# Kernel tuning notes

Hardware: AMD Instinct MI355X
Metric: run time of the kernel (lower is better)

## Reference

```python
import jax, jax.numpy as jnp
import numpy as np

H = 2        # num_heads
C = 128      # in_channels
K_ORDER = 4
BETA = 0.5


def _gcn_conv(x, row, col, deg_inv, n):
    # x: [N, H, C]; adj_t = D^{-1} A^T where A[row, col] = 1
    # (adj_t @ x)[c] = deg_inv[c] * sum_{e: col_e == c} x[row_e]
    msg = x[row]  # [E, H, C]
    agg = jax.ops.segment_sum(msg, col, num_segments=n)  # [N, H, C]
    return agg * deg_inv[:, None, None]


def _attn_conv(qs, ks, vs):
    # linear (kernelized) attention, non-block path
    n = qs.shape[0]
    kvs = jnp.einsum('lhm,lhd->hmd', ks, vs)            # [H, C, C]
    qkvs = jnp.einsum('nhm,hmd->nhd', qs, kvs)          # [N, H, C]
    vs_sum = vs.sum(axis=0)                             # [H, C]
    num = qkvs + vs_sum[None, :, :]
    ks_sum = ks.sum(axis=0)                             # [H, C]
    qks_sum = jnp.einsum('nhm,hm->nh', qs, ks_sum)[:, :, None]  # [N, H, 1]
    den = qks_sum + jnp.asarray(n, qs.dtype)
    return num / den


def setup_inputs() -> dict:
    key = jax.random.key(0)
    ks = jax.random.split(key, 8)
    N, E = 100000, 1600000
    x = jax.random.normal(ks[0], (N, C), jnp.float32)
    edge_index = jax.random.randint(ks[1], (2, E), 0, N, jnp.int64)
    s_in = 1.0 / np.sqrt(C)
    s_out = 1.0 / np.sqrt(H * C * (K_ORDER + 1))
    Wq_w = jax.random.normal(ks[2], (C, H * C), jnp.float32) * s_in
    Wq_b = jax.random.normal(ks[3], (H * C,), jnp.float32) * s_in
    Wk_w = jax.random.normal(ks[4], (C, H * C), jnp.float32) * s_in
    Wk_b = jax.random.normal(ks[5], (H * C,), jnp.float32) * s_in
    Wo_w = jax.random.normal(ks[6], (H * C * (K_ORDER + 1), C), jnp.float32) * s_out
    Wo_b = jax.random.normal(ks[7], (C,), jnp.float32) * s_out
    return {"x": x, "edge_index": edge_index, "Wq_w": Wq_w, "Wq_b": Wq_b,
            "Wk_w": Wk_w, "Wk_b": Wk_b, "Wo_w": Wo_w, "Wo_b": Wo_b}


def reference(x, edge_index, Wq_w, Wq_b, Wk_w, Wk_b, Wo_w, Wo_b):
    n = x.shape[0]
    row, col = edge_index[0], edge_index[1]
    # normalized adjacency D^{-1} A^T (pow(-1.0) in the source, not -0.5)
    deg = jax.ops.segment_sum(jnp.ones(row.shape[0], x.dtype), col, num_segments=n)
    deg_inv = jnp.where(deg > 0, 1.0 / deg, 0.0)

    query = (x @ Wq_w + Wq_b).reshape(n, H, C)
    key = (x @ Wk_w + Wk_b).reshape(n, H, C)
    qs = query / jnp.linalg.norm(query, axis=2, keepdims=True)
    ks = key / jnp.linalg.norm(key, axis=2, keepdims=True)

    x0 = jnp.broadcast_to(x[:, None, :], (n, H, C))  # [N, H, C]
    terms = [x0]
    for _ in range(K_ORDER):
        prev = terms[-1]
        gcn_i = _gcn_conv(prev, row, col, deg_inv, n)
        attn_i = _attn_conv(qs, ks, prev)
        terms.append(BETA * gcn_i + attn_i)
    xcat = jnp.concatenate(terms, axis=-1)  # [N, H, C*(K+1)]
    xcat = xcat.reshape(n, H * C * (K_ORDER + 1))
    return (xcat @ Wo_w + Wo_b) / H
```

## Files before the change

### kernel.cpp

```cpp
#include <hip/hip_runtime.h>

#define THREADS 256
#define NB 512
#define SEGCAP 6144

typedef __attribute__((ext_vector_type(8))) short short8;
typedef __attribute__((ext_vector_type(4))) float f32x4;

__device__ __forceinline__ float bf2f(unsigned short u) {
    union { unsigned int i; float f; } v;
    v.i = ((unsigned int)u) << 16;
    return v.f;
}
__device__ __forceinline__ unsigned short f2bf(float f) {
    union { float f; unsigned int i; } v;
    v.f = f;
    unsigned int r = (v.i + 0x7FFFu + ((v.i >> 16) & 1u)) >> 16;
    return (unsigned short)r;
}
__device__ __forceinline__ float4 ld4f(const float* p) {
    return *reinterpret_cast<const float4*>(p);
}
__device__ __forceinline__ float4 ld4f(const unsigned short* p) {
    ushort4 u = *reinterpret_cast<const ushort4*>(p);
    return make_float4(bf2f(u.x), bf2f(u.y), bf2f(u.z), bf2f(u.w));
}

__device__ __forceinline__ int edge_get(const int* base, int E, int mode, int which, int e) {
    size_t idx = (size_t)which * (size_t)E + (size_t)e;
    return mode ? base[2 * idx] : base[idx];
}

__global__ __launch_bounds__(256) void k_detect(const int* __restrict__ e, int E,
                                                int* __restrict__ mode) {
    __shared__ int nz;
    if (threadIdx.x == 0) nz = 0;
    __syncthreads();
    int lim = 2 * E;
    if (lim > 8192) lim = 8192;
    for (int i = 1 + 2 * (int)threadIdx.x; i < lim; i += 512)
        if (e[i] != 0) nz = 1;
    __syncthreads();
    if (threadIdx.x == 0) *mode = (nz == 0) ? 1 : 0;
}

__global__ __launch_bounds__(256) void k_hist(const int* __restrict__ eb, int E,
                                              const int* __restrict__ mode, int N, int CW, int epb,
                                              int* __restrict__ gcnt) {
    __shared__ int hist[NB];
    for (int i = threadIdx.x; i < NB; i += 256) hist[i] = 0;
    __syncthreads();
    int m = *mode;
    int e0 = blockIdx.x * epb;
    int e1 = min(e0 + epb, E);
    for (int e = e0 + threadIdx.x; e < e1; e += 256) {
        int c = edge_get(eb, E, m, 1, e);
        if ((unsigned)c < (unsigned)N) atomicAdd(&hist[c / CW], 1);
    }
    __syncthreads();
    for (int i = threadIdx.x; i < NB; i += 256)
        if (hist[i]) atomicAdd(&gcnt[i], hist[i]);
}

__global__ __launch_bounds__(NB) void k_bscan(const int* __restrict__ gcnt,
                                              int* __restrict__ gbase, int* __restrict__ gcursor) {
    __shared__ int s[NB];
    int t = threadIdx.x;
    int v = gcnt[t];
    s[t] = v;
    __syncthreads();
    for (int off = 1; off < NB; off <<= 1) {
        int add = (t >= off) ? s[t - off] : 0;
        __syncthreads();
        s[t] += add;
        __syncthreads();
    }
    gbase[t] = s[t] - v;
    gcursor[t] = s[t] - v;
}

__global__ __launch_bounds__(256) void k_part(const int* __restrict__ eb, int E,
                                              const int* __restrict__ mode, int N, int CW, int epb,
                                              int* __restrict__ gcursor, uint2* __restrict__ ebuf) {
    __shared__ int hist[NB];
    __shared__ int base[NB];
    for (int i = threadIdx.x; i < NB; i += 256) hist[i] = 0;
    __syncthreads();
    int m = *mode;
    int e0 = blockIdx.x * epb;
    int e1 = min(e0 + epb, E);
    for (int e = e0 + threadIdx.x; e < e1; e += 256) {
        int c = edge_get(eb, E, m, 1, e);
        if ((unsigned)c < (unsigned)N) atomicAdd(&hist[c / CW], 1);
    }
    __syncthreads();
    for (int i = threadIdx.x; i < NB; i += 256) {
        int h = hist[i];
        base[i] = h ? atomicAdd(&gcursor[i], h) : 0;
        hist[i] = 0;
    }
    __syncthreads();
    for (int e = e0 + threadIdx.x; e < e1; e += 256) {
        int c = edge_get(eb, E, m, 1, e);
        if ((unsigned)c < (unsigned)N) {
            int r = edge_get(eb, E, m, 0, e);
            if ((unsigned)r >= (unsigned)N) r = 0;
            int b = c / CW;
            int li = atomicAdd(&hist[b], 1);
            ebuf[(size_t)base[b] + li] = make_uint2((unsigned)r, (unsigned)c);
        }
    }
}

__global__ __launch_bounds__(256) void k_build(const uint2* __restrict__ ebuf,
                                               const int* __restrict__ gbase,
                                               const int* __restrict__ gcnt, int N, int CW,
                                               int* __restrict__ cnt, int* __restrict__ offs,
                                               float* __restrict__ deg_inv, int* __restrict__ csr) {
    __shared__ int hist[256];
    __shared__ int pfx[256];
    __shared__ int seg[SEGCAP];
    const int b = blockIdx.x;
    const int col0 = b * CW;
    const int ncols = min(CW, N - col0);
    if (ncols <= 0) return;
    const int ebase = gbase[b], ecnt = gcnt[b];
    const int t = threadIdx.x;
    for (int i = t; i < 256; i += 256) hist[i] = 0;
    __syncthreads();
    for (int e = t; e < ecnt; e += 256) {
        uint2 rc = ebuf[(size_t)ebase + e];
        atomicAdd(&hist[rc.y - col0], 1);
    }
    __syncthreads();
    int v = (t < ncols) ? hist[t] : 0;
    pfx[t] = v;
    __syncthreads();
    for (int off = 1; off < 256; off <<= 1) {
        int add = (t >= off) ? pfx[t - off] : 0;
        __syncthreads();
        pfx[t] += add;
        __syncthreads();
    }
    int excl = pfx[t] - v;
    if (t < ncols) {
        cnt[col0 + t] = v;
        offs[col0 + t] = ebase + excl;
        deg_inv[col0 + t] = (v > 0) ? 1.0f / (float)v : 0.0f;
    }
    __syncthreads();
    if (t < 256) hist[t] = (t < ncols) ? excl : 0;
    __syncthreads();
    if (ecnt <= SEGCAP) {
        for (int e = t; e < ecnt; e += 256) {
            uint2 rc = ebuf[(size_t)ebase + e];
            int li = atomicAdd(&hist[rc.y - col0], 1);
            seg[li] = (int)rc.x;
        }
        __syncthreads();
        for (int e = t; e < ecnt; e += 256) csr[(size_t)ebase + e] = seg[e];
    } else {
        for (int e = t; e < ecnt; e += 256) {
            uint2 rc = ebuf[(size_t)ebase + e];
            int li = atomicAdd(&hist[rc.y - col0], 1);
            csr[(size_t)ebase + li] = (int)rc.x;
        }
    }
}

__global__ __launch_bounds__(256) void k_prep_wqk(const float* __restrict__ Wq,
                                                  const float* __restrict__ Wk,
                                                  unsigned short* __restrict__ WqkT) {
    int i = blockIdx.x * 256 + threadIdx.x;
    if (i < 512 * 128) {
        int oc = i >> 7, k = i & 127;
        float v = (oc < 256) ? Wq[k * 256 + oc] : Wk[k * 256 + (oc - 256)];
        WqkT[i] = f2bf(v);
    }
}

__global__ __launch_bounds__(256) void k_prep_wo(const float* __restrict__ Wo,
                                                 unsigned short* __restrict__ WoT) {
    int i = blockIdx.x * 256 + threadIdx.x;
    if (i < 1280 * 128) {
        int r = i >> 7, j = i & 127;
        WoT[(size_t)j * 1280 + r] = f2bf(Wo[i]);
    }
}

__global__ __launch_bounds__(256) void k_proj(const float* __restrict__ x,
                                              const unsigned short* __restrict__ WqkT,
                                              const float* __restrict__ bq,
                                              const float* __restrict__ bk,
                                              unsigned short* __restrict__ qs,
                                              unsigned short* __restrict__ ks, int N) {
    __shared__ unsigned short xs[64 * 128];
    __shared__ unsigned short os[64 * 256];
    const int t = threadIdx.x;
    const int n0 = blockIdx.x * 64;
#pragma unroll
    for (int i = 0; i < 4; i++) {
        int chunk = i * 256 + t;
        int r = chunk >> 4, c0 = (chunk & 15) * 8;
        float4 a0 = make_float4(0.f, 0.f, 0.f, 0.f), a1 = a0;
        if (n0 + r < N) {
            a0 = ld4f(&x[(size_t)(n0 + r) * 128 + c0]);
            a1 = ld4f(&x[(size_t)(n0 + r) * 128 + c0 + 4]);
        }
        short8 v = {(short)f2bf(a0.x), (short)f2bf(a0.y), (short)f2bf(a0.z), (short)f2bf(a0.w),
                    (short)f2bf(a1.x), (short)f2bf(a1.y), (short)f2bf(a1.z), (short)f2bf(a1.w)};
        int byte = r * 256 + ((c0 * 2) ^ ((r & 7) << 4));
        *reinterpret_cast<short8*>(reinterpret_cast<char*>(xs) + byte) = v;
    }
    __syncthreads();
    const int w = t >> 6, l = t & 63, lrow = l & 15, lhi = l >> 4;
    f32x4 acc[4][8];
    const f32x4 fz = {0.f, 0.f, 0.f, 0.f};
#pragma unroll
    for (int mt = 0; mt < 4; mt++)
#pragma unroll
        for (int nt = 0; nt < 8; nt++) acc[mt][nt] = fz;

    for (int kk = 0; kk < 4; kk++) {
        int kb = kk * 32 + lhi * 8;
        short8 af[4];
#pragma unroll
        for (int mt = 0; mt < 4; mt++) {
            int r = mt * 16 + lrow;
            af[mt] = *reinterpret_cast<const short8*>(
                reinterpret_cast<const char*>(xs) + r * 256 + ((kb * 2) ^ ((r & 7) << 4)));
        }
#pragma unroll
        for (int nt = 0; nt < 8; nt++) {
            int oc = w * 128 + nt * 16 + lrow;
            short8 bf = *reinterpret_cast<const short8*>(&WqkT[(size_t)oc * 128 + kb]);
#pragma unroll
            for (int mt = 0; mt < 4; mt++)
                acc[mt][nt] = __builtin_amdgcn_mfma_f32_16x16x32_bf16(af[mt], bf, acc[mt][nt], 0, 0, 0);
        }
    }
#pragma unroll
    for (int nt = 0; nt < 8; nt++) {
        int oc = w * 128 + nt * 16 + lrow;
        float b = (oc < 256) ? bq[oc] : bk[oc - 256];
#pragma unroll
        for (int mt = 0; mt < 4; mt++)
#pragma unroll
            for (int reg = 0; reg < 4; reg++) acc[mt][nt][reg] += b;
    }
    const int hc = (w & 1) * 128;
    float rv[4][4];
#pragma unroll
    for (int mt = 0; mt < 4; mt++) {
        float ss[4] = {0.f, 0.f, 0.f, 0.f};
#pragma unroll
        for (int nt = 0; nt < 8; nt++)
#pragma unroll
            for (int reg = 0; reg < 4; reg++) ss[reg] += acc[mt][nt][reg] * acc[mt][nt][reg];
#pragma unroll
        for (int m_ = 1; m_ < 16; m_ <<= 1)
#pragma unroll
            for (int reg = 0; reg < 4; reg++) ss[reg] += __shfl_xor(ss[reg], m_);
#pragma unroll
        for (int reg = 0; reg < 4; reg++) rv[mt][reg] = rsqrtf(ss[reg]);
    }
    for (int pass = 0; pass < 2; pass++) {
        if ((w >> 1) == pass) {
#pragma unroll
            for (int mt = 0; mt < 4; mt++)
#pragma unroll
                for (int reg = 0; reg < 4; reg++) {
                    int r = mt * 16 + lhi * 4 + reg;
#pragma unroll
                    for (int nt = 0; nt < 8; nt++)
                        os[r * 256 + hc + nt * 16 + lrow] = f2bf(acc[mt][nt][reg] * rv[mt][reg]);
                }
        }
        __syncthreads();
        unsigned short* dstg = pass ? ks : qs;
#pragma unroll
        for (int i = 0; i < 8; i++) {
            int chunk = i * 256 + t;
            int r = chunk >> 5, c = (chunk & 31) * 8;
            int n = n0 + r;
            if (n < N)
                *reinterpret_cast<short8*>(&dstg[(size_t)n * 256 + c]) =
                    *reinterpret_cast<const short8*>(&os[r * 256 + c]);
        }
        __syncthreads();
    }
}

__global__ __launch_bounds__(256) void k_colsum(const unsigned short* __restrict__ ks, int N,
                                                float* __restrict__ part) {
    const int t = threadIdx.x;
    const int stride = (N + 255) >> 8;
    int r0 = blockIdx.x * stride;
    int rend = min(r0 + stride, N);
    float s = 0.f;
    for (int n = r0; n < rend; n++) s += bf2f(ks[(size_t)n * 256 + t]);
    part[blockIdx.x * 256 + t] = s;
}

__global__ __launch_bounds__(256) void k_colsum2(const float* __restrict__ part,
                                                 float* __restrict__ ks_sum) {
    const int t = threadIdx.x;
    float s = 0.f;
    for (int b = 0; b < 256; b++) s += part[b * 256 + t];
    ks_sum[t] = s;
}

__global__ __launch_bounds__(256) void k_den(const unsigned short* __restrict__ qs,
                                             const float* __restrict__ ks_sum,
                                             float* __restrict__ den, int N) {
    int w = threadIdx.x >> 6, lane = threadIdx.x & 63;
    int n = blockIdx.x * 4 + w;
    if (n >= N) return;
    float4 q = ld4f(&qs[(size_t)n * 256 + lane * 4]);
    float4 kv = *reinterpret_cast<const float4*>(&ks_sum[lane * 4]);
    float s = q.x * kv.x + q.y * kv.y + q.z * kv.z + q.w * kv.w;
#pragma unroll
    for (int off = 1; off < 32; off <<= 1) s += __shfl_xor(s, off);
    if ((lane & 31) == 0) den[n * 2 + (lane >> 5)] = s + (float)N;
}

__device__ __forceinline__ short8 frag_ld(const unsigned short* tile, int kb, int col) {
    const char* b = reinterpret_cast<const char*>(tile);
    int cb = (col * 2) ^ (((kb >> 3) & 3) << 5);
    short8 r;
#pragma unroll
    for (int i = 0; i < 8; i++)
        r[i] = (short)*reinterpret_cast<const unsigned short*>(b + (kb + i) * 512 + cb);
    return r;
}

template <typename TV>
__global__ __launch_bounds__(256) void k_kvs2(const unsigned short* __restrict__ ks,
                                              const TV* __restrict__ vs, int vstride, int vmask,
                                              float* __restrict__ partial,
                                              float* __restrict__ pvsum, int rows_per, int N) {
    __shared__ unsigned short kt[32 * 256];
    __shared__ unsigned short vt[32 * 256];
    __shared__ float vred[8][256];
    const int t = threadIdx.x;
    const int w = t >> 6, l = t & 63, lrow = l & 15, lhi = l >> 4;
    const int h = w >> 1, mhalf = w & 1;
    const int r0 = blockIdx.x * rows_per;
    const int rend = min(r0 + rows_per, N);

    const f32x4 fz = {0.f, 0.f, 0.f, 0.f};
    f32x4 acc[4][8];
#pragma unroll
    for (int mt = 0; mt < 4; mt++)
#pragma unroll
        for (int nt = 0; nt < 8; nt++) acc[mt][nt] = fz;
    float vsum8[8] = {0.f, 0.f, 0.f, 0.f, 0.f, 0.f, 0.f, 0.f};

    for (int c0 = r0; c0 < rend; c0 += 32) {
#pragma unroll
        for (int i = 0; i < 4; i++) {
            int chunk = i * 256 + t;
            int n = chunk >> 5, cc = (chunk & 31) * 8;
            short8 v = {0, 0, 0, 0, 0, 0, 0, 0};
            if (c0 + n < rend)
                v = *reinterpret_cast<const short8*>(&ks[(size_t)(c0 + n) * 256 + cc]);
            *reinterpret_cast<short8*>(reinterpret_cast<char*>(kt) + n * 512 +
                                       ((cc * 2) ^ (((n >> 3) & 3) << 5))) = v;
        }
#pragma unroll
        for (int i = 0; i < 4; i++) {
            int chunk = i * 256 + t;
            int n = chunk >> 5, cc = (chunk & 31) * 8;
            float4 a0 = make_float4(0.f, 0.f, 0.f, 0.f), a1 = a0;
            if (c0 + n < rend) {
                a0 = ld4f(&vs[(size_t)(c0 + n) * vstride + (cc & vmask)]);
                a1 = ld4f(&vs[(size_t)(c0 + n) * vstride + ((cc + 4) & vmask)]);
            }
            unsigned short u0 = f2bf(a0.x), u1 = f2bf(a0.y), u2 = f2bf(a0.z), u3 = f2bf(a0.w);
            unsigned short u4 = f2bf(a1.x), u5 = f2bf(a1.y), u6 = f2bf(a1.z), u7 = f2bf(a1.w);
            vsum8[0] += bf2f(u0); vsum8[1] += bf2f(u1); vsum8[2] += bf2f(u2); vsum8[3] += bf2f(u3);
            vsum8[4] += bf2f(u4); vsum8[5] += bf2f(u5); vsum8[6] += bf2f(u6); vsum8[7] += bf2f(u7);
            short8 v = {(short)u0, (short)u1, (short)u2, (short)u3,
                        (short)u4, (short)u5, (short)u6, (short)u7};
            *reinterpret_cast<short8*>(reinterpret_cast<char*>(vt) + n * 512 +
                                       ((cc * 2) ^ (((n >> 3) & 3) << 5))) = v;
        }
        __syncthreads();
        {
            int kb = lhi * 8;
            short8 af[4];
#pragma unroll
            for (int mt = 0; mt < 4; mt++)
                af[mt] = frag_ld(vt, kb, h * 128 + mhalf * 64 + mt * 16 + lrow);
#pragma unroll
            for (int nt = 0; nt < 8; nt++) {
                short8 bf = frag_ld(kt, kb, h * 128 + nt * 16 + lrow);
#pragma unroll
                for (int mt = 0; mt < 4; mt++)
                    acc[mt][nt] =
                        __builtin_amdgcn_mfma_f32_16x16x32_bf16(af[mt], bf, acc[mt][nt], 0, 0, 0);
            }
        }
        __syncthreads();
    }
    float* pb = &partial[((size_t)blockIdx.x * 2 + h) * 16384];
#pragma unroll
    for (int mt = 0; mt < 4; mt++)
#pragma unroll
        for (int reg = 0; reg < 4; reg++) {
            int c_local = mhalf * 64 + mt * 16 + lhi * 4 + reg;
#pragma unroll
            for (int nt = 0; nt < 8; nt++) pb[c_local * 128 + nt * 16 + lrow] = acc[mt][nt][reg];
        }
    {
        int cc = (t & 31) * 8;
#pragma unroll
        for (int j = 0; j < 8; j++) vred[t >> 5][cc + j] = vsum8[j];
        __syncthreads();
        float s = 0.f;
#pragma unroll
        for (int r = 0; r < 8; r++) s += vred[r][t];
        pvsum[blockIdx.x * 256 + t] = s;
    }
}

__global__ __launch_bounds__(256) void k_kvred(const float* __restrict__ partial,
                                               const float* __restrict__ pvsum, int S,
                                               unsigned short* __restrict__ kvsT,
                                               float* __restrict__ vs_sum) {
    if (blockIdx.x == 128) {
        int c = threadIdx.x;
        float s = 0.f;
        for (int i = 0; i < S; i++) s += pvsum[i * 256 + c];
        vs_sum[c] = s;
        return;
    }
    int e = blockIdx.x * 256 + threadIdx.x;
    float s = 0.f;
    for (int i = 0; i < S; i++) s += partial[(size_t)i * 32768 + e];
    kvsT[e] = f2bf(s);
}

__global__ __launch_bounds__(256) void k_gather2(const unsigned short* __restrict__ prev,
                                                 const int* __restrict__ csr_src,
                                                 const int* __restrict__ offs,
                                                 const int* __restrict__ cnt,
                                                 const float* __restrict__ deg_inv,
                                                 unsigned short* __restrict__ cur, int N) {
    const int w = threadIdx.x >> 6, l = threadIdx.x & 63;
    int n = blockIdx.x * 4 + w;
    if (n >= N) return;
    const int start = offs[n], d = cnt[n];
    int e = start;
    const int eend = start + d;
    float a0 = 0.f, a1 = 0.f, a2 = 0.f, a3 = 0.f;
    const int co = l * 4;
    for (; e + 16 <= eend; e += 16) {
        int s[16];
#pragma unroll
        for (int i = 0; i < 16; i++) s[i] = csr_src[e + i];
        ushort4 u[16];
#pragma unroll
        for (int i = 0; i < 16; i++)
            u[i] = *reinterpret_cast<const ushort4*>(&prev[(size_t)s[i] * 256 + co]);
#pragma unroll
        for (int i = 0; i < 16; i++) {
            a0 += bf2f(u[i].x); a1 += bf2f(u[i].y); a2 += bf2f(u[i].z); a3 += bf2f(u[i].w);
        }
    }
    for (; e + 8 <= eend; e += 8) {
        int s[8];
#pragma unroll
        for (int i = 0; i < 8; i++) s[i] = csr_src[e + i];
        ushort4 u[8];
#pragma unroll
        for (int i = 0; i < 8; i++)
            u[i] = *reinterpret_cast<const ushort4*>(&prev[(size_t)s[i] * 256 + co]);
#pragma unroll
        for (int i = 0; i < 8; i++) {
            a0 += bf2f(u[i].x); a1 += bf2f(u[i].y); a2 += bf2f(u[i].z); a3 += bf2f(u[i].w);
        }
    }
    for (; e < eend; e++) {
        ushort4 u = *reinterpret_cast<const ushort4*>(&prev[(size_t)csr_src[e] * 256 + co]);
        a0 += bf2f(u.x); a1 += bf2f(u.y); a2 += bf2f(u.z); a3 += bf2f(u.w);
    }
    float sc = 0.5f * deg_inv[n];
    ushort4 o;
    o.x = f2bf(a0 * sc); o.y = f2bf(a1 * sc); o.z = f2bf(a2 * sc); o.w = f2bf(a3 * sc);
    *reinterpret_cast<ushort4*>(&cur[(size_t)n * 256 + co]) = o;
}

__global__ __launch_bounds__(256) void k_gather2f(const float* __restrict__ prev,
                                                  const int* __restrict__ csr_src,
                                                  const int* __restrict__ offs,
                                                  const int* __restrict__ cnt,
                                                  const float* __restrict__ deg_inv,
                                                  unsigned short* __restrict__ cur, int N) {
    const int w = threadIdx.x >> 6, l = threadIdx.x & 63;
    int n = blockIdx.x * 4 + w;
    if (n >= N) return;
    const int start = offs[n], d = cnt[n];
    int e = start;
    const int eend = start + d;
    float a0 = 0.f, a1 = 0.f;
    const int co = l * 2;
    for (; e + 16 <= eend; e += 16) {
        int s[16];
#pragma unroll
        for (int i = 0; i < 16; i++) s[i] = csr_src[e + i];
        float2 u[16];
#pragma unroll
        for (int i = 0; i < 16; i++)
            u[i] = *reinterpret_cast<const float2*>(&prev[(size_t)s[i] * 128 + co]);
#pragma unroll
        for (int i = 0; i < 16; i++) { a0 += u[i].x; a1 += u[i].y; }
    }
    for (; e + 8 <= eend; e += 8) {
        int s[8];
#pragma unroll
        for (int i = 0; i < 8; i++) s[i] = csr_src[e + i];
        float2 u[8];
#pragma unroll
        for (int i = 0; i < 8; i++)
            u[i] = *reinterpret_cast<const float2*>(&prev[(size_t)s[i] * 128 + co]);
#pragma unroll
        for (int i = 0; i < 8; i++) { a0 += u[i].x; a1 += u[i].y; }
    }
    for (; e < eend; e++) {
        float2 u = *reinterpret_cast<const float2*>(&prev[(size_t)csr_src[e] * 128 + co]);
        a0 += u.x; a1 += u.y;
    }
    float sc = 0.5f * deg_inv[n];
    ushort2 o;
    o.x = f2bf(a0 * sc); o.y = f2bf(a1 * sc);
    *reinterpret_cast<ushort2*>(&cur[(size_t)n * 256 + co]) = o;
    *reinterpret_cast<ushort2*>(&cur[(size_t)n * 256 + 128 + co]) = o;
}

__global__ __launch_bounds__(256) void k_att_out(const unsigned short* __restrict__ qs,
                                                 const unsigned short* __restrict__ kvsT,
                                                 const float* __restrict__ vs_sum,
                                                 const float* __restrict__ den,
                                                 unsigned short* __restrict__ cur,
                                                 const unsigned short* __restrict__ WoT,
                                                 float* __restrict__ out, int tblk, int writeCur,
                                                 int N) {
    __shared__ unsigned short sm[64 * 256];
    const int t = threadIdx.x;
    const int n0 = blockIdx.x * 64;
#pragma unroll
    for (int i = 0; i < 8; i++) {
        int chunk = i * 256 + t;
        int r = chunk >> 5, c0 = (chunk & 31) * 8;
        short8 v = {0, 0, 0, 0, 0, 0, 0, 0};
        if (n0 + r < N) v = *reinterpret_cast<const short8*>(&qs[(size_t)(n0 + r) * 256 + c0]);
        *reinterpret_cast<short8*>(reinterpret_cast<char*>(sm) + r * 512 +
                                   ((c0 * 2) ^ ((r & 7) << 4))) = v;
    }
    short8 cv[8];
#pragma unroll
    for (int i = 0; i < 8; i++) {
        int chunk = i * 256 + t;
        int r = chunk >> 5, c0 = (chunk & 31) * 8;
        short8 v = {0, 0, 0, 0, 0, 0, 0, 0};
        if (n0 + r < N) v = *reinterpret_cast<const short8*>(&cur[(size_t)(n0 + r) * 256 + c0]);
        cv[i] = v;
    }
    __syncthreads();
    const int w = t >> 6, l = t & 63, lrow = l & 15, lhi = l >> 4;
    const int h = w >> 1, jh = w & 1;
    const f32x4 fz = {0.f, 0.f, 0.f, 0.f};
    f32x4 acc[4][4];
#pragma unroll
    for (int mt = 0; mt < 4; mt++)
#pragma unroll
        for (int nt = 0; nt < 4; nt++) acc[mt][nt] = fz;

    for (int kk = 0; kk < 4; kk++) {
        int kb = kk * 32 + lhi * 8;
        short8 af[4];
#pragma unroll
        for (int mt = 0; mt < 4; mt++) {
            int r = mt * 16 + lrow;
            af[mt] = *reinterpret_cast<const short8*>(
                reinterpret_cast<const char*>(sm) + r * 512 +
                (((h * 128 + kb) * 2) ^ ((r & 7) << 4)));
        }
#pragma unroll
        for (int nt = 0; nt < 4; nt++) {
            int c = jh * 64 + nt * 16 + lrow;
            short8 bf = *reinterpret_cast<const short8*>(&kvsT[((size_t)h * 128 + c) * 128 + kb]);
#pragma unroll
            for (int mt = 0; mt < 4; mt++)
                acc[mt][nt] = __builtin_amdgcn_mfma_f32_16x16x32_bf16(af[mt], bf, acc[mt][nt], 0, 0, 0);
        }
    }
    __syncthreads();
#pragma unroll
    for (int i = 0; i < 8; i++) {
        int chunk = i * 256 + t;
        int r = chunk >> 5, c0 = (chunk & 31) * 8;
        *reinterpret_cast<short8*>(reinterpret_cast<char*>(sm) + r * 512 +
                                   ((c0 * 2) ^ ((r & 7) << 4))) = cv[i];
    }
    __syncthreads();
#pragma unroll
    for (int mt = 0; mt < 4; mt++) {
#pragma unroll
        for (int reg = 0; reg < 4; reg++) {
            int r = mt * 16 + lhi * 4 + reg;
            int n = n0 + r;
            if (n < N) {
                float idn = 1.0f / den[n * 2 + h];
#pragma unroll
                for (int nt = 0; nt < 4; nt++) {
                    int c = h * 128 + jh * 64 + nt * 16 + lrow;
                    unsigned short* sp = reinterpret_cast<unsigned short*>(
                        reinterpret_cast<char*>(sm) + r * 512 + ((c * 2) ^ ((r & 7) << 4)));
                    float v = bf2f(*sp) + (acc[mt][nt][reg] + vs_sum[c]) * idn;
                    *sp = f2bf(v);
                }
            }
        }
    }
    __syncthreads();
    if (writeCur) {
#pragma unroll
        for (int i = 0; i < 8; i++) {
            int chunk = i * 256 + t;
            int r = chunk >> 5, c0 = (chunk & 31) * 8;
            int n = n0 + r;
            if (n < N)
                *reinterpret_cast<short8*>(&cur[(size_t)n * 256 + c0]) =
                    *reinterpret_cast<const short8*>(reinterpret_cast<const char*>(sm) + r * 512 +
                                                     ((c0 * 2) ^ ((r & 7) << 4)));
        }
    }
    f32x4 acc2[4][2];
#pragma unroll
    for (int mt = 0; mt < 4; mt++)
#pragma unroll
        for (int nt = 0; nt < 2; nt++) acc2[mt][nt] = fz;
    for (int kk = 0; kk < 8; kk++) {
        int kb = kk * 32 + lhi * 8;
        short8 af[4];
#pragma unroll
        for (int mt = 0; mt < 4; mt++) {
            int r = mt * 16 + lrow;
            af[mt] = *reinterpret_cast<const short8*>(
                reinterpret_cast<const char*>(sm) + r * 512 + ((kb * 2) ^ ((r & 7) << 4)));
        }
        int woff = (kb >> 7) * 640 + tblk * 128 + (kb & 127);
#pragma unroll
        for (int nt = 0; nt < 2; nt++) {
            int j = w * 32 + nt * 16 + lrow;
            short8 bf = *reinterpret_cast<const short8*>(&WoT[(size_t)j * 1280 + woff]);
#pragma unroll
            for (int mt = 0; mt < 4; mt++)
                acc2[mt][nt] = __builtin_amdgcn_mfma_f32_16x16x32_bf16(af[mt], bf, acc2[mt][nt], 0, 0, 0);
        }
    }
#pragma unroll
    for (int nt = 0; nt < 2; nt++) {
        int j = w * 32 + nt * 16 + lrow;
#pragma unroll
        for (int mt = 0; mt < 4; mt++)
#pragma unroll
            for (int reg = 0; reg < 4; reg++) {
                int n = n0 + mt * 16 + lhi * 4 + reg;
                if (n < N) out[(size_t)n * 128 + j] += 0.5f * acc2[mt][nt][reg];
            }
    }
}

__global__ __launch_bounds__(256) void k_out0(const float* __restrict__ x,
                                              const unsigned short* __restrict__ WoT,
                                              const float* __restrict__ Wo_b,
                                              float* __restrict__ out, int N) {
    __shared__ unsigned short sm[64 * 256];
    const int t = threadIdx.x;
    const int n0 = blockIdx.x * 64;
#pragma unroll
    for (int i = 0; i < 8; i++) {
        int chunk = i * 256 + t;
        int r = chunk >> 5, c0 = (chunk & 31) * 8, cs = c0 & 127;
        float4 a0 = make_float4(0.f, 0.f, 0.f, 0.f), a1 = a0;
        if (n0 + r < N) {
            a0 = ld4f(&x[(size_t)(n0 + r) * 128 + cs]);
            a1 = ld4f(&x[(size_t)(n0 + r) * 128 + cs + 4]);
        }
        short8 v = {(short)f2bf(a0.x), (short)f2bf(a0.y), (short)f2bf(a0.z), (short)f2bf(a0.w),
                    (short)f2bf(a1.x), (short)f2bf(a1.y), (short)f2bf(a1.z), (short)f2bf(a1.w)};
        *reinterpret_cast<short8*>(reinterpret_cast<char*>(sm) + r * 512 +
                                   ((c0 * 2) ^ ((r & 7) << 4))) = v;
    }
    __syncthreads();
    const int w = t >> 6, l = t & 63, lrow = l & 15, lhi = l >> 4;
    const f32x4 fz = {0.f, 0.f, 0.f, 0.f};
    f32x4 acc2[4][2];
#pragma unroll
    for (int mt = 0; mt < 4; mt++)
#pragma unroll
        for (int nt = 0; nt < 2; nt++) acc2[mt][nt] = fz;
    for (int kk = 0; kk < 8; kk++) {
        int kb = kk * 32 + lhi * 8;
        short8 af[4];
#pragma unroll
        for (int mt = 0; mt < 4; mt++) {
            int r = mt * 16 + lrow;
            af[mt] = *reinterpret_cast<const short8*>(
                reinterpret_cast<const char*>(sm) + r * 512 + ((kb * 2) ^ ((r & 7) << 4)));
        }
        int woff = (kb >> 7) * 640 + (kb & 127);
#pragma unroll
        for (int nt = 0; nt < 2; nt++) {
            int j = w * 32 + nt * 16 + lrow;
            short8 bf = *reinterpret_cast<const short8*>(&WoT[(size_t)j * 1280 + woff]);
#pragma unroll
            for (int mt = 0; mt < 4; mt++)
                acc2[mt][nt] = __builtin_amdgcn_mfma_f32_16x16x32_bf16(af[mt], bf, acc2[mt][nt], 0, 0, 0);
        }
    }
#pragma unroll
    for (int nt = 0; nt < 2; nt++) {
        int j = w * 32 + nt * 16 + lrow;
        float b = Wo_b[j];
#pragma unroll
        for (int mt = 0; mt < 4; mt++)
#pragma unroll
            for (int reg = 0; reg < 4; reg++) {
                int n = n0 + mt * 16 + lhi * 4 + reg;
                if (n < N) out[(size_t)n * 128 + j] = 0.5f * (acc2[mt][nt][reg] + b);
            }
    }
}

extern "C" void kernel_launch(void* const* d_in, const int* in_sizes, int n_in,
                              void* d_out, int out_size, void* d_ws, size_t ws_size,
                              hipStream_t stream) {
    const int N = in_sizes[0] / 128;
    const int E = in_sizes[1] / 2;
    const float* x = (const float*)d_in[0];
    const int* eraw = (const int*)d_in[1];
    const float* Wq_w = (const float*)d_in[2];
    const float* Wq_b = (const float*)d_in[3];
    const float* Wk_w = (const float*)d_in[4];
    const float* Wk_b = (const float*)d_in[5];
    const float* Wo_w = (const float*)d_in[6];
    const float* Wo_b = (const float*)d_in[7];
    float* out = (float*)d_out;

    char* p = (char*)d_ws;
    auto alloc = [&](size_t bytes) -> void* {
        void* r = (void*)p;
        p += (bytes + 255) & ~(size_t)255;
        return r;
    };
    unsigned short* qs = (unsigned short*)alloc((size_t)N * 256 * 2);
    unsigned short* ks = (unsigned short*)alloc((size_t)N * 256 * 2);
    unsigned short* bufA = (unsigned short*)alloc((size_t)N * 256 * 2);
    unsigned short* bufB = (unsigned short*)alloc((size_t)N * 256 * 2);
    float* deg_inv = (float*)alloc((size_t)N * 4);
    float* den = (float*)alloc((size_t)N * 2 * 4);
    float* ks_sum = (float*)alloc(256 * 4);
    float* vs_sum = (float*)alloc(256 * 4);
    float* colpart = (float*)alloc(256 * 256 * 4);
    unsigned short* WqkT = (unsigned short*)alloc(512 * 128 * 2);
    unsigned short* WoT = (unsigned short*)alloc(1280 * 128 * 2);
    unsigned short* kvsTb = (unsigned short*)alloc(32768 * 2);
    int* cnt = (int*)alloc((size_t)N * 4);
    int* offs = (int*)alloc((size_t)N * 4);
    int* gcnt = (int*)alloc(NB * 4);
    int* gbase = (int*)alloc(NB * 4);
    int* gcursor = (int*)alloc(NB * 4);
    int* mode = (int*)alloc(256);
    int* csr = (int*)alloc((size_t)E * 4);
    uint2* ebuf = (uint2*)alloc((size_t)E * 8);

    size_t used = (size_t)(p - (char*)d_ws);
    size_t rem = (ws_size > used + (1 << 20)) ? ws_size - used - (1 << 20) : 0;
    int S = (int)(rem / (32768 * 4 + 1024));
    if (S > 512) S = 512;
    if (S < 8) S = 8;
    float* partial = (float*)alloc((size_t)S * 32768 * 4);
    float* pvsum = (float*)alloc((size_t)S * 256 * 4);
    const int rows_per = (N + S - 1) / S;

    const int CW = (N + NB - 1) / NB;
    const int EBLK = 256;
    const int epb = (E + EBLK - 1) / EBLK;

    hipMemsetAsync(gcnt, 0, NB * 4, stream);

    k_detect<<<1, 256, 0, stream>>>(eraw, E, mode);
    k_hist<<<EBLK, 256, 0, stream>>>(eraw, E, mode, N, CW, epb, gcnt);
    k_bscan<<<1, NB, 0, stream>>>(gcnt, gbase, gcursor);
    k_part<<<EBLK, 256, 0, stream>>>(eraw, E, mode, N, CW, epb, gcursor, ebuf);
    k_build<<<NB, 256, 0, stream>>>(ebuf, gbase, gcnt, N, CW, cnt, offs, deg_inv, csr);

    k_prep_wqk<<<256, 256, 0, stream>>>(Wq_w, Wk_w, WqkT);
    k_prep_wo<<<640, 256, 0, stream>>>(Wo_w, WoT);

    const int nb64 = (N + 63) / 64;
    k_proj<<<nb64, 256, 0, stream>>>(x, WqkT, Wq_b, Wk_b, qs, ks, N);
    k_colsum<<<256, 256, 0, stream>>>(ks, N, colpart);
    k_colsum2<<<1, 256, 0, stream>>>(colpart, ks_sum);
    k_den<<<(N + 3) / 4, 256, 0, stream>>>(qs, ks_sum, den, N);
    k_out0<<<nb64, 256, 0, stream>>>(x, WoT, Wo_b, out, N);

    const int gb4 = (N + 3) / 4;

    k_kvs2<float><<<S, 256, 0, stream>>>(ks, x, 128, 127, partial, pvsum, rows_per, N);
    k_kvred<<<129, 256, 0, stream>>>(partial, pvsum, S, kvsTb, vs_sum);
    k_gather2f<<<gb4, 256, 0, stream>>>(x, csr, offs, cnt, deg_inv, bufA, N);
    k_att_out<<<nb64, 256, 0, stream>>>(qs, kvsTb, vs_sum, den, bufA, WoT, out, 1, 1, N);

    unsigned short* prev = bufA;
    unsigned short* cur = bufB;
    for (int step = 2; step <= 4; step++) {
        k_kvs2<unsigned short><<<S, 256, 0, stream>>>(ks, prev, 256, 255, partial, pvsum, rows_per,
                                                      N);
        k_kvred<<<129, 256, 0, stream>>>(partial, pvsum, S, kvsTb, vs_sum);
        k_gather2<<<gb4, 256, 0, stream>>>(prev, csr, offs, cnt, deg_inv, cur, N);
        k_att_out<<<nb64, 256, 0, stream>>>(qs, kvsTb, vs_sum, den, cur, WoT, out, step,
                                            (step < 4) ? 1 : 0, N);
        unsigned short* tmp = prev;
        prev = cur;
        cur = tmp;
    }
}
```

Before: 1.857 ms.

## Batch output projection into two flush kernels and pre-sum x0 weight blocks

```diff
diff --git a/kernel.cpp b/kernel.cpp
--- a/kernel.cpp
+++ b/kernel.cpp
@@ -185,6 +185,15 @@
     if (i < 1280 * 128) {
         int r = i >> 7, j = i & 127;
         WoT[(size_t)j * 1280 + r] = f2bf(Wo[i]);
+    }
+}
+
+__global__ __launch_bounds__(256) void k_prep_wo0(const float* __restrict__ Wo,
+                                                  unsigned short* __restrict__ WoT0) {
+    int i = blockIdx.x * 256 + threadIdx.x;
+    if (i < 16384) {
+        int j = i >> 7, c = i & 127;
+        WoT0[i] = f2bf(Wo[(size_t)c * 128 + j] + Wo[(size_t)(640 + c) * 128 + j]);
     }
 }
 
@@ -436,9 +445,20 @@
         return;
     }
     int e = blockIdx.x * 256 + threadIdx.x;
-    float s = 0.f;
-    for (int i = 0; i < S; i++) s += partial[(size_t)i * 32768 + e];
-    kvsT[e] = f2bf(s);
+    float s0 = 0.f, s1 = 0.f, s2 = 0.f, s3 = 0.f, s4 = 0.f, s5 = 0.f, s6 = 0.f, s7 = 0.f;
+    int i = 0;
+    for (; i + 8 <= S; i += 8) {
+        s0 += partial[(size_t)(i + 0) * 32768 + e];
+        s1 += partial[(size_t)(i + 1) * 32768 + e];
+        s2 += partial[(size_t)(i + 2) * 32768 + e];
+        s3 += partial[(size_t)(i + 3) * 32768 + e];
+        s4 += partial[(size_t)(i + 4) * 32768 + e];
+        s5 += partial[(size_t)(i + 5) * 32768 + e];
+        s6 += partial[(size_t)(i + 6) * 32768 + e];
+        s7 += partial[(size_t)(i + 7) * 32768 + e];
+    }
+    for (; i < S; i++) s0 += partial[(size_t)i * 32768 + e];
+    kvsT[e] = f2bf(((s0 + s1) + (s2 + s3)) + ((s4 + s5) + (s6 + s7)));
 }
 
 __global__ __launch_bounds__(256) void k_gather2(const unsigned short* __restrict__ prev,
@@ -542,10 +562,7 @@
                                                  const unsigned short* __restrict__ kvsT,
                                                  const float* __restrict__ vs_sum,
                                                  const float* __restrict__ den,
-                                                 unsigned short* __restrict__ cur,
-                                                 const unsigned short* __restrict__ WoT,
-                                                 float* __restrict__ out, int tblk, int writeCur,
-                                                 int N) {
+                                                 unsigned short* __restrict__ cur, int N) {
     __shared__ unsigned short sm[64 * 256];
     const int t = threadIdx.x;
     const int n0 = blockIdx.x * 64;
@@ -598,14 +615,6 @@
     }
     __syncthreads();
 #pragma unroll
-    for (int i = 0; i < 8; i++) {
-        int chunk = i * 256 + t;
-        int r = chunk >> 5, c0 = (chunk & 31) * 8;
-        *reinterpret_cast<short8*>(reinterpret_cast<char*>(sm) + r * 512 +
-                                   ((c0 * 2) ^ ((r & 7) << 4))) = cv[i];
-    }
-    __syncthreads();
-#pragma unroll
     for (int mt = 0; mt < 4; mt++) {
 #pragma unroll
         for (int reg = 0; reg < 4; reg++) {
@@ -618,120 +627,137 @@
                     int c = h * 128 + jh * 64 + nt * 16 + lrow;
                     unsigned short* sp = reinterpret_cast<unsigned short*>(
                         reinterpret_cast<char*>(sm) + r * 512 + ((c * 2) ^ ((r & 7) << 4)));
-                    float v = bf2f(*sp) + (acc[mt][nt][reg] + vs_sum[c]) * idn;
-                    *sp = f2bf(v);
+                    *sp = f2bf((acc[mt][nt][reg] + vs_sum[c]) * idn);
                 }
             }
         }
     }
     __syncthreads();
-    if (writeCur) {
+#pragma unroll
+    for (int i = 0; i < 8; i++) {
+        int chunk = i * 256 + t;
+        int r = chunk >> 5, c0 = (chunk & 31) * 8;
+        int n = n0 + r;
+        if (n < N) {
+            short8 a = *reinterpret_cast<const short8*>(reinterpret_cast<const char*>(sm) +
+                                                        r * 512 + ((c0 * 2) ^ ((r & 7) << 4)));
+            short8 o;
+#pragma unroll
+            for (int j = 0; j < 8; j++)
+                o[j] = (short)f2bf(bf2f((unsigned short)cv[i][j]) + bf2f((unsigned short)a[j]));
+            *reinterpret_cast<short8*>(&cur[(size_t)n * 256 + c0]) = o;
+        }
+    }
+}
+
+template <int FIRST>
+__global__ __launch_bounds__(256) void k_outflush(const float* __restrict__ x,
+                                                  const unsigned short* __restrict__ ta,
+                                                  const unsigned short* __restrict__ tb,
+                                                  const unsigned short* __restrict__ WoT,
+                                                  const unsigned short* __restrict__ WoT0,
+                                                  const float* __restrict__ Wo_b,
+                                                  float* __restrict__ out, int tblkA, int tblkB,
+                                                  int N) {
+    __shared__ unsigned short sm[64 * 256];
+    const int t = threadIdx.x;
+    const int n0 = blockIdx.x * 64;
+    const int w = t >> 6, l = t & 63, lrow = l & 15, lhi = l >> 4;
+    const f32x4 fz = {0.f, 0.f, 0.f, 0.f};
+    f32x4 acc2[4][2];
+#pragma unroll
+    for (int mt = 0; mt < 4; mt++)
+#pragma unroll
+        for (int nt = 0; nt < 2; nt++) acc2[mt][nt] = fz;
+
+    if (FIRST) {
+#pragma unroll
+        for (int i = 0; i < 4; i++) {
+            int chunk = i * 256 + t;
+            int r = chunk >> 4, c0 = (chunk & 15) * 8;
+            float4 a0 = make_float4(0.f, 0.f, 0.f, 0.f), a1 = a0;
+            if (n0 + r < N) {
+                a0 = ld4f(&x[(size_t)(n0 + r) * 128 + c0]);
+                a1 = ld4f(&x[(size_t)(n0 + r) * 128 + c0 + 4]);
+            }
+            short8 v = {(short)f2bf(a0.x), (short)f2bf(a0.y), (short)f2bf(a0.z), (short)f2bf(a0.w),
+                        (short)f2bf(a1.x), (short)f2bf(a1.y), (short)f2bf(a1.z), (short)f2bf(a1.w)};
+            *reinterpret_cast<short8*>(reinterpret_cast<char*>(sm) + r * 256 +
+                                       ((c0 * 2) ^ ((r & 7) << 4))) = v;
+        }
+        __syncthreads();
+        for (int kk = 0; kk < 4; kk++) {
+            int kb = kk * 32 + lhi * 8;
+            short8 af[4];
+#pragma unroll
+            for (int mt = 0; mt < 4; mt++) {
+                int r = mt * 16 + lrow;
+                af[mt] = *reinterpret_cast<const short8*>(
+                    reinterpret_cast<const char*>(sm) + r * 256 + ((kb * 2) ^ ((r & 7) << 4)));
+            }
+#pragma unroll
+            for (int nt = 0; nt < 2; nt++) {
+                int j = w * 32 + nt * 16 + lrow;
+                short8 bf = *reinterpret_cast<const short8*>(&WoT0[(size_t)j * 128 + kb]);
+#pragma unroll
+                for (int mt = 0; mt < 4; mt++)
+                    acc2[mt][nt] =
+                        __builtin_amdgcn_mfma_f32_16x16x32_bf16(af[mt], bf, acc2[mt][nt], 0, 0, 0);
+            }
+        }
+        __syncthreads();
+    }
+#pragma unroll
+    for (int b = 0; b < 2; b++) {
+        const unsigned short* buf = b ? tb : ta;
+        const int tblk = b ? tblkB : tblkA;
 #pragma unroll
         for (int i = 0; i < 8; i++) {
             int chunk = i * 256 + t;
             int r = chunk >> 5, c0 = (chunk & 31) * 8;
-            int n = n0 + r;
-            if (n < N)
-                *reinterpret_cast<short8*>(&cur[(size_t)n * 256 + c0]) =
-                    *reinterpret_cast<const short8*>(reinterpret_cast<const char*>(sm) + r * 512 +
-                                                     ((c0 * 2) ^ ((r & 7) << 4)));
-        }
-    }
-    f32x4 acc2[4][2];
-#pragma unroll
-    for (int mt = 0; mt < 4; mt++)
-#pragma unroll
-        for (int nt = 0; nt < 2; nt++) acc2[mt][nt] = fz;
-    for (int kk = 0; kk < 8; kk++) {
-        int kb = kk * 32 + lhi * 8;
-        short8 af[4];
-#pragma unroll
-        for (int mt = 0; mt < 4; mt++) {
-            int r = mt * 16 + lrow;
-            af[mt] = *reinterpret_cast<const short8*>(
-                reinterpret_cast<const char*>(sm) + r * 512 + ((kb * 2) ^ ((r & 7) << 4)));
-        }
-        int woff = (kb >> 7) * 640 + tblk * 128 + (kb & 127);
-#pragma unroll
-        for (int nt = 0; nt < 2; nt++) {
-            int j = w * 32 + nt * 16 + lrow;
-            short8 bf = *reinterpret_cast<const short8*>(&WoT[(size_t)j * 1280 + woff]);
-#pragma unroll
-            for (int mt = 0; mt < 4; mt++)
-                acc2[mt][nt] = __builtin_amdgcn_mfma_f32_16x16x32_bf16(af[mt], bf, acc2[mt][nt], 0, 0, 0);
-        }
+            short8 v = {0, 0, 0, 0, 0, 0, 0, 0};
+            if (n0 + r < N) v = *reinterpret_cast<const short8*>(&buf[(size_t)(n0 + r) * 256 + c0]);
+            *reinterpret_cast<short8*>(reinterpret_cast<char*>(sm) + r * 512 +
+                                       ((c0 * 2) ^ ((r & 7) << 4))) = v;
+        }
+        __syncthreads();
+        for (int kk = 0; kk < 8; kk++) {
+            int kb = kk * 32 + lhi * 8;
+            short8 af[4];
+#pragma unroll
+            for (int mt = 0; mt < 4; mt++) {
+                int r = mt * 16 + lrow;
+                af[mt] = *reinterpret_cast<const short8*>(
+                    reinterpret_cast<const char*>(sm) + r * 512 + ((kb * 2) ^ ((r & 7) << 4)));
+            }
+            int woff = (kb >> 7) * 640 + tblk * 128 + (kb & 127);
+#pragma unroll
+            for (int nt = 0; nt < 2; nt++) {
+                int j = w * 32 + nt * 16 + lrow;
+                short8 bf = *reinterpret_cast<const short8*>(&WoT[(size_t)j * 1280 + woff]);
+#pragma unroll
+                for (int mt = 0; mt < 4; mt++)
+                    acc2[mt][nt] =
+                        __builtin_amdgcn_mfma_f32_16x16x32_bf16(af[mt], bf, acc2[mt][nt], 0, 0, 0);
+            }
+        }
+        __syncthreads();
     }
 #pragma unroll
     for (int nt = 0; nt < 2; nt++) {
         int j = w * 32 + nt * 16 + lrow;
+        float b = FIRST ? Wo_b[j] : 0.f;
 #pragma unroll
         for (int mt = 0; mt < 4; mt++)
 #pragma unroll
             for (int reg = 0; reg < 4; reg++) {
                 int n = n0 + mt * 16 + lhi * 4 + reg;
-                if (n < N) out[(size_t)n * 128 + j] += 0.5f * acc2[mt][nt][reg];
-            }
-    }
-}
-
-__global__ __launch_bounds__(256) void k_out0(const float* __restrict__ x,
-                                              const unsigned short* __restrict__ WoT,
-                                              const float* __restrict__ Wo_b,
-                                              float* __restrict__ out, int N) {
-    __shared__ unsigned short sm[64 * 256];
-    const int t = threadIdx.x;
-    const int n0 = blockIdx.x * 64;
-#pragma unroll
-    for (int i = 0; i < 8; i++) {
-        int chunk = i * 256 + t;
-        int r = chunk >> 5, c0 = (chunk & 31) * 8, cs = c0 & 127;
-        float4 a0 = make_float4(0.f, 0.f, 0.f, 0.f), a1 = a0;
-        if (n0 + r < N) {
-            a0 = ld4f(&x[(size_t)(n0 + r) * 128 + cs]);
-            a1 = ld4f(&x[(size_t)(n0 + r) * 128 + cs + 4]);
-        }
-        short8 v = {(short)f2bf(a0.x), (short)f2bf(a0.y), (short)f2bf(a0.z), (short)f2bf(a0.w),
-                    (short)f2bf(a1.x), (short)f2bf(a1.y), (short)f2bf(a1.z), (short)f2bf(a1.w)};
-        *reinterpret_cast<short8*>(reinterpret_cast<char*>(sm) + r * 512 +
-                                   ((c0 * 2) ^ ((r & 7) << 4))) = v;
-    }
-    __syncthreads();
-    const int w = t >> 6, l = t & 63, lrow = l & 15, lhi = l >> 4;
-    const f32x4 fz = {0.f, 0.f, 0.f, 0.f};
-    f32x4 acc2[4][2];
-#pragma unroll
-    for (int mt = 0; mt < 4; mt++)
-#pragma unroll
-        for (int nt = 0; nt < 2; nt++) acc2[mt][nt] = fz;
-    for (int kk = 0; kk < 8; kk++) {
-        int kb = kk * 32 + lhi * 8;
-        short8 af[4];
-#pragma unroll
-        for (int mt = 0; mt < 4; mt++) {
-            int r = mt * 16 + lrow;
-            af[mt] = *reinterpret_cast<const short8*>(
-                reinterpret_cast<const char*>(sm) + r * 512 + ((kb * 2) ^ ((r & 7) << 4)));
-        }
-        int woff = (kb >> 7) * 640 + (kb & 127);
-#pragma unroll
-        for (int nt = 0; nt < 2; nt++) {
-            int j = w * 32 + nt * 16 + lrow;
-            short8 bf = *reinterpret_cast<const short8*>(&WoT[(size_t)j * 1280 + woff]);
-#pragma unroll
-            for (int mt = 0; mt < 4; mt++)
-                acc2[mt][nt] = __builtin_amdgcn_mfma_f32_16x16x32_bf16(af[mt], bf, acc2[mt][nt], 0, 0, 0);
-        }
-    }
-#pragma unroll
-    for (int nt = 0; nt < 2; nt++) {
-        int j = w * 32 + nt * 16 + lrow;
-        float b = Wo_b[j];
-#pragma unroll
-        for (int mt = 0; mt < 4; mt++)
-#pragma unroll
-            for (int reg = 0; reg < 4; reg++) {
-                int n = n0 + mt * 16 + lhi * 4 + reg;
-                if (n < N) out[(size_t)n * 128 + j] = 0.5f * (acc2[mt][nt][reg] + b);
+                if (n < N) {
+                    if (FIRST)
+                        out[(size_t)n * 128 + j] = 0.5f * (acc2[mt][nt][reg] + b);
+                    else
+                        out[(size_t)n * 128 + j] += 0.5f * acc2[mt][nt][reg];
+                }
             }
     }
 }
@@ -768,6 +794,7 @@
     float* colpart = (float*)alloc(256 * 256 * 4);
     unsigned short* WqkT = (unsigned short*)alloc(512 * 128 * 2);
     unsigned short* WoT = (unsigned short*)alloc(1280 * 128 * 2);
+    unsigned short* WoT0 = (unsigned short*)alloc(128 * 128 * 2);
     unsigned short* kvsTb = (unsigned short*)alloc(32768 * 2);
     int* cnt = (int*)alloc((size_t)N * 4);
     int* offs = (int*)alloc((size_t)N * 4);
@@ -781,7 +808,7 @@
     size_t used = (size_t)(p - (char*)d_ws);
     size_t rem = (ws_size > used + (1 << 20)) ? ws_size - used - (1 << 20) : 0;
     int S = (int)(rem / (32768 * 4 + 1024));
-    if (S > 512) S = 512;
+    if (S > 256) S = 256;
     if (S < 8) S = 8;
     float* partial = (float*)alloc((size_t)S * 32768 * 4);
     float* pvsum = (float*)alloc((size_t)S * 256 * 4);
@@ -801,32 +828,37 @@
 
     k_prep_wqk<<<256, 256, 0, stream>>>(Wq_w, Wk_w, WqkT);
     k_prep_wo<<<640, 256, 0, stream>>>(Wo_w, WoT);
+    k_prep_wo0<<<64, 256, 0, stream>>>(Wo_w, WoT0);
 
     const int nb64 = (N + 63) / 64;
     k_proj<<<nb64, 256, 0, stream>>>(x, WqkT, Wq_b, Wk_b, qs, ks, N);
     k_colsum<<<256, 256, 0, stream>>>(ks, N, colpart);
     k_colsum2<<<1, 256, 0, stream>>>(colpart, ks_sum);
     k_den<<<(N + 3) / 4, 256, 0, stream>>>(qs, ks_sum, den, N);
-    k_out0<<<nb64, 256, 0, stream>>>(x, WoT, Wo_b, out, N);
 
     const int gb4 = (N + 3) / 4;
 
     k_kvs2<float><<<S, 256, 0, stream>>>(ks, x, 128, 127, partial, pvsum, rows_per, N);
     k_kvred<<<129, 256, 0, stream>>>(partial, pvsum, S, kvsTb, vs_sum);
     k_gather2f<<<gb4, 256, 0, stream>>>(x, csr, offs, cnt, deg_inv, bufA, N);
-    k_att_out<<<nb64, 256, 0, stream>>>(qs, kvsTb, vs_sum, den, bufA, WoT, out, 1, 1, N);
-
-    unsigned short* prev = bufA;
-    unsigned short* cur = bufB;
-    for (int step = 2; step <= 4; step++) {
-        k_kvs2<unsigned short><<<S, 256, 0, stream>>>(ks, prev, 256, 255, partial, pvsum, rows_per,
-                                                      N);
-        k_kvred<<<129, 256, 0, stream>>>(partial, pvsum, S, kvsTb, vs_sum);
-        k_gather2<<<gb4, 256, 0, stream>>>(prev, csr, offs, cnt, deg_inv, cur, N);
-        k_att_out<<<nb64, 256, 0, stream>>>(qs, kvsTb, vs_sum, den, cur, WoT, out, step,
-                                            (step < 4) ? 1 : 0, N);
-        unsigned short* tmp = prev;
-        prev = cur;
-        cur = tmp;
-    }
-}
+    k_att_out<<<nb64, 256, 0, stream>>>(qs, kvsTb, vs_sum, den, bufA, N);
+
+    k_kvs2<unsigned short><<<S, 256, 0, stream>>>(ks, bufA, 256, 255, partial, pvsum, rows_per, N);
+    k_kvred<<<129, 256, 0, stream>>>(partial, pvsum, S, kvsTb, vs_sum);
+    k_gather2<<<gb4, 256, 0, stream>>>(bufA, csr, offs, cnt, deg_inv, bufB, N);
+    k_att_out<<<nb64, 256, 0, stream>>>(qs, kvsTb, vs_sum, den, bufB, N);
+
+    k_outflush<1><<<nb64, 256, 0, stream>>>(x, bufA, bufB, WoT, WoT0, Wo_b, out, 1, 2, N);
+
+    k_kvs2<unsigned short><<<S, 256, 0, stream>>>(ks, bufB, 256, 255, partial, pvsum, rows_per, N);
+    k_kvred<<<129, 256, 0, stream>>>(partial, pvsum, S, kvsTb, vs_sum);
+    k_gather2<<<gb4, 256, 0, stream>>>(bufB, csr, offs, cnt, deg_inv, bufA, N);
+    k_att_out<<<nb64, 256, 0, stream>>>(qs, kvsTb, vs_sum, den, bufA, N);
+
+    k_kvs2<unsigned short><<<S, 256, 0, stream>>>(ks, bufA, 256, 255, partial, pvsum, rows_per, N);
+    k_kvred<<<129, 256, 0, stream>>>(partial, pvsum, S, kvsTb, vs_sum);
+    k_gather2<<<gb4, 256, 0, stream>>>(bufA, csr, offs, cnt, deg_inv, bufB, N);
+    k_att_out<<<nb64, 256, 0, stream>>>(qs, kvsTb, vs_sum, den, bufB, N);
+
+    k_outflush<0><<<nb64, 256, 0, stream>>>(x, bufA, bufB, WoT, WoT0, Wo_b, out, 3, 4, N);
+}
```

New measurement: 1.637 ms. 1.13x faster.
